# Kernel optimization log

Measured on AMD Instinct MI355X. Metric: run time of the kernel, lower is better.

Reference implementation:

```python
import jax, jax.numpy as jnp
import numpy as np

BETA = 0.04
EPS_LOW = 0.2
EPS_HIGH = 0.2
KL_PERCENTILE = 0.2
TEMPERATURE = 1.0


def setup_inputs() -> dict:
    key = jax.random.key(0)
    k1, k2, k3, k4, k5, k6 = jax.random.split(key, 6)
    B, T, H, V = 8, 512, 1024, 32000
    scale = 0.02  # keep logits / log-ratios numerically sane
    return {
        "_input": jax.random.normal(k1, (B, T, H), jnp.float32) * scale,
        "lin_weight": jax.random.normal(k2, (V, H), jnp.float32) * scale,
        "selected_token_ids": jax.random.randint(k3, (B, T), 0, V, jnp.int32),
        "attention_mask": jnp.ones((B, T), jnp.float32),
        "advantages": jax.random.normal(k4, (B,), jnp.float32),
        "ref_input": jax.random.normal(k5, (B, T, H), jnp.float32) * scale,
        "ref_weight": jax.random.normal(k6, (V, H), jnp.float32) * scale,
    }


def _per_token_logps(x, w, ids):
    # x: [B,T,H], w: [V,H] -> log_softmax(logits/temp) gathered at ids -> [B,T]
    logits = jnp.einsum("bth,vh->btv", x, w) / TEMPERATURE
    logps = jax.nn.log_softmax(logits, axis=-1)
    return jnp.take_along_axis(logps, ids[..., None], axis=-1)[..., 0]


def _k3_percentile(log_p, log_q, percentile):
    # kthvalue over the whole batch of log_p (k-th smallest)
    flat = log_p.reshape(-1)
    n = flat.shape[0]
    k = max(1, int(n * percentile))
    threshold = jnp.sort(flat)[k - 1]
    mask = (log_p <= threshold).astype(log_p.dtype)
    log_ratio = log_p - log_q
    k3 = jnp.exp(log_ratio) - log_ratio - 1.0
    scale = 1.0 / percentile if percentile > 0 else 1.0
    return mask * k3 * scale


def reference(_input, lin_weight, selected_token_ids, attention_mask, advantages,
              ref_input, ref_weight):
    per_token_logps = _per_token_logps(_input, lin_weight, selected_token_ids)
    ref_per_token_logps = jax.lax.stop_gradient(
        _per_token_logps(ref_input, ref_weight, selected_token_ids))
    old_per_token_logps = jax.lax.stop_gradient(per_token_logps)

    # token-level importance sampling
    log_iw = per_token_logps - old_per_token_logps  # [B,T]
    coef_1 = jnp.exp(log_iw)
    coef_2 = jnp.clip(coef_1, 1.0 - EPS_LOW, 1.0 + EPS_HIGH)
    adv = advantages[:, None]  # [B,1]
    per_token_loss = -jnp.minimum(coef_1 * adv, coef_2 * adv)

    kl_div = _k3_percentile(ref_per_token_logps, per_token_logps, KL_PERCENTILE)
    per_token_loss = per_token_loss + BETA * kl_div

    # loss_type == 'dapo': normalize by total unmasked tokens (full batch)
    full_attention_mask = attention_mask
    normalizer = jnp.clip(full_attention_mask.sum(), 1.0, None)
    loss = (per_token_loss * attention_mask).sum() / normalizer

    kl_metric = (kl_div * attention_mask).sum() / jnp.clip(full_attention_mask.sum(), 1.0, None)
    is_clipped = ((coef_1 < 1.0 - EPS_LOW) & (adv < 0)) | ((coef_1 > 1.0 + EPS_HIGH) & (adv > 0))
    clip_ratio = (is_clipped.astype(jnp.float32) * attention_mask).sum() / jnp.clip(
        full_attention_mask.sum(), 1.0, None)
    return loss, kl_metric, clip_ratio
```

## Files before the change

### kernel.cpp

```cpp
#include <hip/hip_runtime.h>
#include <hip/hip_bf16.h>

typedef __bf16 bf16_t;
typedef __bf16 bf16x4 __attribute__((ext_vector_type(4)));
typedef __bf16 bf16x8 __attribute__((ext_vector_type(8)));
typedef float f32x4 __attribute__((ext_vector_type(4)));

#define NTOK 4096
#define TT   512
#define HH   1024
#define VV   32000

#define BM 256
#define BN 256
#define BK 64
#define NKT 16

#define GLOBAL_AS(p) ((const __attribute__((address_space(1))) void*)(const void*)(p))
#define LDS_AS(p)    ((__attribute__((address_space(3))) void*)(void*)(p))

__global__ __launch_bounds__(256)
void grpo_cvt_all(const float* __restrict__ X,  const float* __restrict__ W,
                  const float* __restrict__ Xr, const float* __restrict__ Wr,
                  bf16_t* __restrict__ Xb,  bf16_t* __restrict__ Wb,
                  bf16_t* __restrict__ Xrb, bf16_t* __restrict__ Wrb)
{
    const int nX4 = NTOK * HH / 4;
    const int nW4 = VV * HH / 4;
    const int b1 = nX4, b2 = nX4 + nW4, b3 = nX4 + nW4 + nX4;
    const int total = 2 * (nX4 + nW4);
    const int stride = gridDim.x * 256;
    for (int i = blockIdx.x * 256 + threadIdx.x; i < total; i += stride) {
        const float* s; bf16_t* d; int j;
        if      (i < b1) { s = X;  d = Xb;  j = i; }
        else if (i < b2) { s = W;  d = Wb;  j = i - b1; }
        else if (i < b3) { s = Xr; d = Xrb; j = i - b2; }
        else             { s = Wr; d = Wrb; j = i - b3; }
        f32x4 v = *(const f32x4*)(s + (size_t)j * 4);
        bf16x4 b;
#pragma unroll
        for (int e = 0; e < 4; ++e) b[e] = (bf16_t)v[e];
        *(bf16x4*)(d + (size_t)j * 4) = b;
    }
}

template<int SBUF, int SMAT, int SKH>
__device__ __forceinline__ void stage_region(bf16_t* lds0, const bf16_t* __restrict__ src,
                                             int kc, int tid, int wid)
{
    bf16_t* reg = lds0 + ((SBUF * 2 + SMAT) * 2 + SKH) * 8192;
#pragma unroll
    for (int i = 0; i < 2; ++i) {
        const int f     = i * 512 + tid;
        const int lslot = (f & 3) ^ ((f >> 3) & 3);
        const bf16_t* g = src + (size_t)(f >> 2) * HH + kc + lslot * 8;
        bf16_t* l = reg + (i * 512 + wid * 64) * 8;
        __builtin_amdgcn_global_load_lds(GLOBAL_AS(g), LDS_AS(l), 16, 0, 0);
    }
}

template<int RBUF, int RKH, int SBUF, int SKH, int SOFF>
__device__ __forceinline__ void phase(f32x4 (&acc)[8][4], bf16_t* lds0,
                                      const bf16_t* pA, const bf16_t* pB,
                                      const bf16_t* __restrict__ gA,
                                      const bf16_t* __restrict__ gB,
                                      int te, int tid, int wid)
{
    constexpr int ra = ((RBUF * 2 + 0) * 2 + RKH) * 8192;
    constexpr int rb = ((RBUF * 2 + 1) * 2 + RKH) * 8192;

    bf16x8 fa[8], fb[4];
#pragma unroll
    for (int m = 0; m < 8; ++m)
        fa[m] = *(const bf16x8*)(pA + ra + m * 16 * 32);
#pragma unroll
    for (int n = 0; n < 4; ++n)
        fb[n] = *(const bf16x8*)(pB + rb + n * 16 * 32);

    {
        const int kc = ((te + SOFF) & (NKT - 1)) * BK + SKH * 32;
        stage_region<SBUF, 0, SKH>(lds0, gA, kc, tid, wid);
        stage_region<SBUF, 1, SKH>(lds0, gB, kc, tid, wid);
    }

    asm volatile("s_waitcnt lgkmcnt(0)" ::: "memory");
    __builtin_amdgcn_sched_barrier(0);

    __builtin_amdgcn_s_setprio(1);
#pragma unroll
    for (int m = 0; m < 8; ++m)
#pragma unroll
        for (int n = 0; n < 4; ++n)
            acc[m][n] = __builtin_amdgcn_mfma_f32_16x16x32_bf16(
                fa[m], fb[n], acc[m][n], 0, 0, 0);
    __builtin_amdgcn_s_setprio(0);

    asm volatile("s_waitcnt vmcnt(4)" ::: "memory");
    asm volatile("s_barrier" ::: "memory");
}

__global__ __launch_bounds__(512)
void grpo_gemm4(const bf16_t* __restrict__ Xb,  const bf16_t* __restrict__ Wb,
                const bf16_t* __restrict__ Xrb, const bf16_t* __restrict__ Wrb,
                const int* __restrict__ ids,
                float* __restrict__ S_p, float* __restrict__ SEL_p,
                float* __restrict__ S_r, float* __restrict__ SEL_r)
{
    __shared__ bf16_t lds[2][2][2][256][32];
    bf16_t* lds0 = &lds[0][0][0][0][0];

    const int tid  = threadIdx.x;
    const int lane = tid & 63;
    const int wid  = tid >> 6;
    const int wr   = wid >> 2;
    const int wc   = wid & 3;
    const int l16  = lane & 15;
    const int g    = lane >> 4;
    const int ps   = g ^ ((l16 >> 1) & 3);
    const bf16_t* pA = lds0 + (wr * 128 + l16) * 32 + ps * 8;
    const bf16_t* pB = lds0 + (wc * 64 + l16) * 32 + ps * 8;

    const int zz = blockIdx.z;
    const bf16_t* Xs = zz ? Xrb : Xb;
    const bf16_t* Ws = zz ? Wrb : Wb;
    float* S   = zz ? S_r   : S_p;
    float* SEL = zz ? SEL_r : SEL_p;

    const int m0 = blockIdx.x * BM;
    const int n0 = blockIdx.y * BN;

    const bf16_t* gA = Xs + (size_t)m0 * HH;
    const bf16_t* gB = Ws + (size_t)n0 * HH;

    f32x4 acc[8][4];
#pragma unroll
    for (int m = 0; m < 8; ++m)
#pragma unroll
        for (int n = 0; n < 4; ++n)
            acc[m][n] = (f32x4)0.0f;

    stage_region<0, 0, 0>(lds0, gA, 0,  tid, wid);
    stage_region<0, 1, 0>(lds0, gB, 0,  tid, wid);
    stage_region<0, 0, 1>(lds0, gA, 32, tid, wid);
    stage_region<0, 1, 1>(lds0, gB, 32, tid, wid);
    stage_region<1, 0, 0>(lds0, gA, 64, tid, wid);
    stage_region<1, 1, 0>(lds0, gB, 64, tid, wid);
    asm volatile("s_waitcnt vmcnt(8)" ::: "memory");
    asm volatile("s_barrier" ::: "memory");

#pragma unroll 1
    for (int it = 0, te = 0; it < NKT / 2; ++it, te += 2) {
        phase<0, 0,  1, 1,  1>(acc, lds0, pA, pB, gA, gB, te, tid, wid);
        phase<0, 1,  0, 0,  2>(acc, lds0, pA, pB, gA, gB, te, tid, wid);
        phase<1, 0,  0, 1,  2>(acc, lds0, pA, pB, gA, gB, te, tid, wid);
        phase<1, 1,  1, 0,  3>(acc, lds0, pA, pB, gA, gB, te, tid, wid);
    }
    asm volatile("s_waitcnt vmcnt(0) lgkmcnt(0)" ::: "memory");
    asm volatile("s_barrier" ::: "memory");

#pragma unroll
    for (int m = 0; m < 8; ++m) {
#pragma unroll
        for (int j = 0; j < 4; ++j) {
            int row = m0 + wr * 128 + m * 16 + g * 4 + j;
            float s = 0.f;
#pragma unroll
            for (int n = 0; n < 4; ++n)
                s += __expf(acc[m][n][j]);
            s += __shfl_xor(s, 1, 64);
            s += __shfl_xor(s, 2, 64);
            s += __shfl_xor(s, 4, 64);
            s += __shfl_xor(s, 8, 64);
            if (l16 == 0) atomicAdd(&S[row], s);

            int id   = ids[row];
            int base = n0 + wc * 64 + l16;
#pragma unroll
            for (int n = 0; n < 4; ++n)
                if (id == base + n * 16) SEL[row] = acc[m][n][j];
        }
    }
}

__global__ void grpo_init(float* __restrict__ p)
{
    p[blockIdx.x * 1024 + threadIdx.x] = 0.f;
}

__global__ __launch_bounds__(1024)
void grpo_prep(const float* __restrict__ S_p, const float* __restrict__ S_r,
               float* __restrict__ lp_p, float* __restrict__ lp_r)
{
    int i = blockIdx.x * 1024 + threadIdx.x;
    lp_p[i] = lp_p[i] - logf(S_p[i]);
    lp_r[i] = lp_r[i] - logf(S_r[i]);
}

__global__ __launch_bounds__(64)
void grpo_thresh(const float* __restrict__ lp_r, float* __restrict__ thr)
{
    __shared__ float sh[NTOK];
    for (int i = threadIdx.x; i < NTOK; i += 64) sh[i] = lp_r[i];
    __syncthreads();
    const float v = sh[blockIdx.x * 64 + threadIdx.x];
    int lt = 0, eq = 0;
#pragma unroll 4
    for (int j = 0; j < NTOK; ++j) {
        float u = sh[j];
        lt += (u < v);
        eq += (u == v);
    }
    if (lt <= 818 && 818 < lt + eq) thr[0] = v;
}

__global__ __launch_bounds__(1024)
void grpo_final(const float* __restrict__ lp_p, const float* __restrict__ lp_r,
                const float* __restrict__ thr,
                const float* __restrict__ am, const float* __restrict__ adv,
                float* __restrict__ out)
{
    __shared__ double red[3][16];
    const int tid = threadIdx.x;
    const float t = thr[0];

    double s_loss = 0.0, s_kl = 0.0, s_am = 0.0;
    for (int i = tid; i < NTOK; i += 1024) {
        float a  = am[i];
        float pr = lp_r[i], pp = lp_p[i];
        float lr = pr - pp;
        float k3 = expf(lr) - lr - 1.0f;
        float kl = (pr <= t) ? k3 * 5.0f : 0.0f;
        float ad = adv[i / TT];
        float ptl = -ad + 0.04f * kl;
        s_loss += (double)(ptl * a);
        s_kl   += (double)(kl * a);
        s_am   += (double)a;
    }
#pragma unroll
    for (int off = 32; off; off >>= 1) {
        s_loss += __shfl_down(s_loss, off, 64);
        s_kl   += __shfl_down(s_kl,   off, 64);
        s_am   += __shfl_down(s_am,   off, 64);
    }
    const int wid = tid >> 6;
    if ((tid & 63) == 0) { red[0][wid] = s_loss; red[1][wid] = s_kl; red[2][wid] = s_am; }
    __syncthreads();
    if (tid == 0) {
        double L = 0, K = 0, A = 0;
        for (int w = 0; w < 16; ++w) { L += red[0][w]; K += red[1][w]; A += red[2][w]; }
        double norm = A < 1.0 ? 1.0 : A;
        out[0] = (float)(L / norm);
        out[1] = (float)(K / norm);
        out[2] = 0.0f;
    }
}

extern "C" void kernel_launch(void* const* d_in, const int* in_sizes, int n_in,
                              void* d_out, int out_size, void* d_ws, size_t ws_size,
                              hipStream_t stream)
{
    const float* X   = (const float*)d_in[0];
    const float* W   = (const float*)d_in[1];
    const int*   ids = (const int*)  d_in[2];
    const float* am  = (const float*)d_in[3];
    const float* adv = (const float*)d_in[4];
    const float* Xr  = (const float*)d_in[5];
    const float* Wr  = (const float*)d_in[6];
    float* out = (float*)d_out;

    float* S_p  = (float*)d_ws;
    float* S_r  = S_p + NTOK;
    float* lp_p = S_r + NTOK;
    float* lp_r = lp_p + NTOK;
    float* thr  = S_p;

    const size_t bf16_off = 65536;
    const size_t nX = (size_t)NTOK * HH, nW = (size_t)VV * HH;

    bf16_t* Xb  = (bf16_t*)((char*)d_ws + bf16_off);
    bf16_t* Wb  = Xb + nX;
    bf16_t* Xrb = Wb + nW;
    bf16_t* Wrb = Xrb + nX;

    hipLaunchKernelGGL(grpo_init, dim3(8), dim3(1024), 0, stream, S_p);

    hipLaunchKernelGGL(grpo_cvt_all, dim3(4096), dim3(256), 0, stream,
                       X, W, Xr, Wr, Xb, Wb, Xrb, Wrb);

    dim3 grid(NTOK / BM, VV / BN, 2);
    hipLaunchKernelGGL(grpo_gemm4, grid, dim3(512), 0, stream,
                       Xb, Wb, Xrb, Wrb, ids, S_p, lp_p, S_r, lp_r);

    hipLaunchKernelGGL(grpo_prep,   dim3(4),  dim3(1024), 0, stream, S_p, S_r, lp_p, lp_r);
    hipLaunchKernelGGL(grpo_thresh, dim3(64), dim3(64),   0, stream, lp_r, thr);
    hipLaunchKernelGGL(grpo_final,  dim3(1),  dim3(1024), 0, stream, lp_p, lp_r, thr, am, adv, out);
}
```

Baseline: 837.1 us.

## Restructure GEMM mainloop into 8-phase interleaved pipeline with full-K64 LDS tiles

Replaces the 4-phase double-buffered K-half pipeline with an 8-phase schedule per K-tile pair. Each phase reads two A fragments and reuses B fragments held in registers across all four phases, interleaving global_load_lds staging of the next tiles between MFMA batches. The LDS layout changes to 64-wide rows with an 8-way XOR swizzle, and each wave covers a different sub-tile mapping. This aims to hide global and LDS latency behind MFMA work and reduce LDS read pressure. The cost is many more barriers per K step, which can stall waves.

```diff
diff --git a/kernel.cpp b/kernel.cpp
--- a/kernel.cpp
+++ b/kernel.cpp
@@ -18,6 +18,11 @@
 
 #define GLOBAL_AS(p) ((const __attribute__((address_space(1))) void*)(const void*)(p))
 #define LDS_AS(p)    ((__attribute__((address_space(3))) void*)(void*)(p))
+
+#define BAR()   asm volatile("s_barrier" ::: "memory")
+#define LGKM0() asm volatile("s_waitcnt lgkmcnt(0)" ::: "memory")
+#define VM4()   asm volatile("s_waitcnt vmcnt(4)" ::: "memory")
+#define SB0()   __builtin_amdgcn_sched_barrier(0)
 
 __global__ __launch_bounds__(256)
 void grpo_cvt_all(const float* __restrict__ X,  const float* __restrict__ W,
@@ -44,70 +49,67 @@
     }
 }
 
-template<int SBUF, int SMAT, int SKH>
-__device__ __forceinline__ void stage_region(bf16_t* lds0, const bf16_t* __restrict__ src,
-                                             int kc, int tid, int wid)
-{
-    bf16_t* reg = lds0 + ((SBUF * 2 + SMAT) * 2 + SKH) * 8192;
+template<int BUF, int MAT, int HALF>
+__device__ __forceinline__ void stage_half(bf16_t* lds0, const bf16_t* __restrict__ src,
+                                           int kc, int tid, int wid)
+{
+    bf16_t* reg = lds0 + (BUF * 4 + MAT * 2 + HALF) * 8192;
 #pragma unroll
     for (int i = 0; i < 2; ++i) {
         const int f     = i * 512 + tid;
-        const int lslot = (f & 3) ^ ((f >> 3) & 3);
-        const bf16_t* g = src + (size_t)(f >> 2) * HH + kc + lslot * 8;
+        const int row   = f >> 3;
+        const int lslot = (f & 7) ^ (row & 7);
+        const bf16_t* g = src + (size_t)(HALF * 128 + row) * HH + kc + lslot * 8;
         bf16_t* l = reg + (i * 512 + wid * 64) * 8;
         __builtin_amdgcn_global_load_lds(GLOBAL_AS(g), LDS_AS(l), 16, 0, 0);
     }
 }
 
-template<int RBUF, int RKH, int SBUF, int SKH, int SOFF>
-__device__ __forceinline__ void phase(f32x4 (&acc)[8][4], bf16_t* lds0,
-                                      const bf16_t* pA, const bf16_t* pB,
-                                      const bf16_t* __restrict__ gA,
-                                      const bf16_t* __restrict__ gB,
-                                      int te, int tid, int wid)
-{
-    constexpr int ra = ((RBUF * 2 + 0) * 2 + RKH) * 8192;
-    constexpr int rb = ((RBUF * 2 + 1) * 2 + RKH) * 8192;
-
-    bf16x8 fa[8], fb[4];
-#pragma unroll
-    for (int m = 0; m < 8; ++m)
-        fa[m] = *(const bf16x8*)(pA + ra + m * 16 * 32);
-#pragma unroll
-    for (int n = 0; n < 4; ++n)
-        fb[n] = *(const bf16x8*)(pB + rb + n * 16 * 32);
-
-    {
-        const int kc = ((te + SOFF) & (NKT - 1)) * BK + SKH * 32;
-        stage_region<SBUF, 0, SKH>(lds0, gA, kc, tid, wid);
-        stage_region<SBUF, 1, SKH>(lds0, gB, kc, tid, wid);
-    }
-
-    asm volatile("s_waitcnt lgkmcnt(0)" ::: "memory");
-    __builtin_amdgcn_sched_barrier(0);
-
-    __builtin_amdgcn_s_setprio(1);
-#pragma unroll
-    for (int m = 0; m < 8; ++m)
-#pragma unroll
-        for (int n = 0; n < 4; ++n)
-            acc[m][n] = __builtin_amdgcn_mfma_f32_16x16x32_bf16(
-                fa[m], fb[n], acc[m][n], 0, 0, 0);
-    __builtin_amdgcn_s_setprio(0);
-
-    asm volatile("s_waitcnt vmcnt(4)" ::: "memory");
-    asm volatile("s_barrier" ::: "memory");
+template<int BUF>
+__device__ __forceinline__ void read_b(const bf16_t* pbk0, const bf16_t* pbk1,
+                                       bf16x8 (&bq)[2][4])
+{
+#pragma unroll
+    for (int n = 0; n < 4; ++n) {
+        bq[0][n] = *(const bf16x8*)(pbk0 + BUF * 32768 + n * 1024);
+        bq[1][n] = *(const bf16x8*)(pbk1 + BUF * 32768 + n * 1024);
+    }
+}
+
+template<int BUF, int MP>
+__device__ __forceinline__ void read_a(const bf16_t* pak0, const bf16_t* pak1,
+                                       bf16x8 (&aq)[2][2])
+{
+#pragma unroll
+    for (int i = 0; i < 2; ++i) {
+        aq[0][i] = *(const bf16x8*)(pak0 + BUF * 32768 + (MP * 2 + i) * 1024);
+        aq[1][i] = *(const bf16x8*)(pak1 + BUF * 32768 + (MP * 2 + i) * 1024);
+    }
+}
+
+template<int MP>
+__device__ __forceinline__ void mfma16(f32x4 (&acc)[8][4],
+                                       bf16x8 (&aq)[2][2], bf16x8 (&bq)[2][4])
+{
+#pragma unroll
+    for (int kh = 0; kh < 2; ++kh)
+#pragma unroll
+        for (int i = 0; i < 2; ++i)
+#pragma unroll
+            for (int n = 0; n < 4; ++n)
+                acc[MP * 2 + i][n] = __builtin_amdgcn_mfma_f32_16x16x32_bf16(
+                    aq[kh][i], bq[kh][n], acc[MP * 2 + i][n], 0, 0, 0);
 }
 
 __global__ __launch_bounds__(512)
-void grpo_gemm4(const bf16_t* __restrict__ Xb,  const bf16_t* __restrict__ Wb,
-                const bf16_t* __restrict__ Xrb, const bf16_t* __restrict__ Wrb,
-                const int* __restrict__ ids,
-                float* __restrict__ S_p, float* __restrict__ SEL_p,
-                float* __restrict__ S_r, float* __restrict__ SEL_r)
-{
-    __shared__ bf16_t lds[2][2][2][256][32];
-    bf16_t* lds0 = &lds[0][0][0][0][0];
+void grpo_gemm_t(const bf16_t* __restrict__ Xb,  const bf16_t* __restrict__ Wb,
+                 const bf16_t* __restrict__ Xrb, const bf16_t* __restrict__ Wrb,
+                 const int* __restrict__ ids,
+                 float* __restrict__ S_p, float* __restrict__ SEL_p,
+                 float* __restrict__ S_r, float* __restrict__ SEL_r)
+{
+    __shared__ bf16_t lds[8][8192];
+    bf16_t* lds0 = &lds[0][0];
 
     const int tid  = threadIdx.x;
     const int lane = tid & 63;
@@ -116,9 +118,16 @@
     const int wc   = wid & 3;
     const int l16  = lane & 15;
     const int g    = lane >> 4;
-    const int ps   = g ^ ((l16 >> 1) & 3);
-    const bf16_t* pA = lds0 + (wr * 128 + l16) * 32 + ps * 8;
-    const bf16_t* pB = lds0 + (wc * 64 + l16) * 32 + ps * 8;
+    const int sw   = l16 & 7;
+
+    const int offA0 = l16 * 64 + ((g ^ sw) * 8);
+    const int offA1 = l16 * 64 + (((g + 4) ^ sw) * 8);
+    const int offB0 = ((wc & 1) * 64 + l16) * 64 + ((g ^ sw) * 8);
+    const int offB1 = ((wc & 1) * 64 + l16) * 64 + (((g + 4) ^ sw) * 8);
+    const bf16_t* pak0 = lds0 + wr * 8192 + offA0;
+    const bf16_t* pak1 = lds0 + wr * 8192 + offA1;
+    const bf16_t* pbk0 = lds0 + 16384 + (wc >> 1) * 8192 + offB0;
+    const bf16_t* pbk1 = lds0 + 16384 + (wc >> 1) * 8192 + offB1;
 
     const int zz = blockIdx.z;
     const bf16_t* Xs = zz ? Xrb : Xb;
@@ -128,7 +137,6 @@
 
     const int m0 = blockIdx.x * BM;
     const int n0 = blockIdx.y * BN;
-
     const bf16_t* gA = Xs + (size_t)m0 * HH;
     const bf16_t* gB = Ws + (size_t)n0 * HH;
 
@@ -139,24 +147,67 @@
         for (int n = 0; n < 4; ++n)
             acc[m][n] = (f32x4)0.0f;
 
-    stage_region<0, 0, 0>(lds0, gA, 0,  tid, wid);
-    stage_region<0, 1, 0>(lds0, gB, 0,  tid, wid);
-    stage_region<0, 0, 1>(lds0, gA, 32, tid, wid);
-    stage_region<0, 1, 1>(lds0, gB, 32, tid, wid);
-    stage_region<1, 0, 0>(lds0, gA, 64, tid, wid);
-    stage_region<1, 1, 0>(lds0, gB, 64, tid, wid);
-    asm volatile("s_waitcnt vmcnt(8)" ::: "memory");
-    asm volatile("s_barrier" ::: "memory");
+    stage_half<0, 1, 0>(lds0, gB, 0,  tid, wid);
+    stage_half<0, 1, 1>(lds0, gB, 0,  tid, wid);
+    stage_half<0, 0, 0>(lds0, gA, 0,  tid, wid);
+    stage_half<0, 0, 1>(lds0, gA, 0,  tid, wid);
+    stage_half<1, 1, 0>(lds0, gB, 64, tid, wid);
+    stage_half<1, 1, 1>(lds0, gB, 64, tid, wid);
+    VM4();
+    BAR();
 
 #pragma unroll 1
     for (int it = 0, te = 0; it < NKT / 2; ++it, te += 2) {
-        phase<0, 0,  1, 1,  1>(acc, lds0, pA, pB, gA, gB, te, tid, wid);
-        phase<0, 1,  0, 0,  2>(acc, lds0, pA, pB, gA, gB, te, tid, wid);
-        phase<1, 0,  0, 1,  2>(acc, lds0, pA, pB, gA, gB, te, tid, wid);
-        phase<1, 1,  1, 0,  3>(acc, lds0, pA, pB, gA, gB, te, tid, wid);
+        const int k1 = ((te + 1) & (NKT - 1)) * BK;
+        const int k2 = ((te + 2) & (NKT - 1)) * BK;
+        const int k3 = ((te + 3) & (NKT - 1)) * BK;
+        bf16x8 aq[2][2], bq[2][4];
+
+        read_b<0>(pbk0, pbk1, bq);
+        read_a<0, 0>(pak0, pak1, aq);
+        stage_half<1, 0, 0>(lds0, gA, k1, tid, wid);
+        BAR(); LGKM0(); SB0();
+        __builtin_amdgcn_s_setprio(1); mfma16<0>(acc, aq, bq); __builtin_amdgcn_s_setprio(0);
+        BAR();
+        read_a<0, 1>(pak0, pak1, aq);
+        stage_half<1, 0, 1>(lds0, gA, k1, tid, wid);
+        stage_half<0, 1, 0>(lds0, gB, k2, tid, wid);
+        BAR(); LGKM0(); SB0();
+        __builtin_amdgcn_s_setprio(1); mfma16<1>(acc, aq, bq); __builtin_amdgcn_s_setprio(0);
+        BAR();
+        read_a<0, 2>(pak0, pak1, aq);
+        stage_half<0, 1, 1>(lds0, gB, k2, tid, wid);
+        BAR(); LGKM0(); SB0();
+        __builtin_amdgcn_s_setprio(1); mfma16<2>(acc, aq, bq); __builtin_amdgcn_s_setprio(0);
+        BAR();
+        read_a<0, 3>(pak0, pak1, aq);
+        BAR(); LGKM0(); SB0();
+        __builtin_amdgcn_s_setprio(1); mfma16<3>(acc, aq, bq); __builtin_amdgcn_s_setprio(0);
+        VM4(); BAR();
+        read_b<1>(pbk0, pbk1, bq);
+        read_a<1, 0>(pak0, pak1, aq);
+        stage_half<0, 0, 0>(lds0, gA, k2, tid, wid);
+        BAR(); LGKM0(); SB0();
+        __builtin_amdgcn_s_setprio(1); mfma16<0>(acc, aq, bq); __builtin_amdgcn_s_setprio(0);
+        BAR();
+        read_a<1, 1>(pak0, pak1, aq);
+        stage_half<0, 0, 1>(lds0, gA, k2, tid, wid);
+        stage_half<1, 1, 0>(lds0, gB, k3, tid, wid);
+        BAR(); LGKM0(); SB0();
+        __builtin_amdgcn_s_setprio(1); mfma16<1>(acc, aq, bq); __builtin_amdgcn_s_setprio(0);
+        BAR();
+        read_a<1, 2>(pak0, pak1, aq);
+        stage_half<1, 1, 1>(lds0, gB, k3, tid, wid);
+        BAR(); LGKM0(); SB0();
+        __builtin_amdgcn_s_setprio(1); mfma16<2>(acc, aq, bq); __builtin_amdgcn_s_setprio(0);
+        BAR();
+        read_a<1, 3>(pak0, pak1, aq);
+        BAR(); LGKM0(); SB0();
+        __builtin_amdgcn_s_setprio(1); mfma16<3>(acc, aq, bq); __builtin_amdgcn_s_setprio(0);
+        VM4(); BAR();
     }
     asm volatile("s_waitcnt vmcnt(0) lgkmcnt(0)" ::: "memory");
-    asm volatile("s_barrier" ::: "memory");
+    BAR();
 
 #pragma unroll
     for (int m = 0; m < 8; ++m) {
@@ -288,7 +339,7 @@
                        X, W, Xr, Wr, Xb, Wb, Xrb, Wrb);
 
     dim3 grid(NTOK / BM, VV / BN, 2);
-    hipLaunchKernelGGL(grpo_gemm4, grid, dim3(512), 0, stream,
+    hipLaunchKernelGGL(grpo_gemm_t, grid, dim3(512), 0, stream,
                        Xb, Wb, Xrb, Wrb, ids, S_p, lp_p, S_r, lp_r);
 
     hipLaunchKernelGGL(grpo_prep,   dim3(4),  dim3(1024), 0, stream, S_p, S_r, lp_p, lp_r);
```

After: 836.0 us. No clear change (-0.1%).
